# Performance work log

Measured on AMD Instinct MI355X. Metric: run time of the kernel, lower is better.

Reference implementation:

```python
import jax, jax.numpy as jnp
import numpy as np

B = 32768   # batch
D = 64      # latent_dimension_half
H = 256     # inner_dimension
T = D * (D + 1) // 2  # 2080 triangular outputs


def setup_inputs() -> dict:
    key = jax.random.key(0)
    ks = jax.random.split(key, 7)
    s = 0.05
    return {
        "x": jax.random.normal(ks[0], (B, D), dtype=jnp.float32),
        "W1": jax.random.normal(ks[1], (D, H), dtype=jnp.float32) * s,
        "b1": jax.random.normal(ks[2], (H,), dtype=jnp.float32) * s,
        "W2": jax.random.normal(ks[3], (H, H), dtype=jnp.float32) * s,
        "b2": jax.random.normal(ks[4], (H,), dtype=jnp.float32) * s,
        "W3": jax.random.normal(ks[5], (H, T), dtype=jnp.float32) * s,
        "b3": jax.random.normal(ks[6], (T,), dtype=jnp.float32) * s,
    }


def reference(x, W1, b1, W2, b2, W3, b3):
    d = x.shape[-1]  # latent_dimension_half
    h = jnp.tanh(x @ W1 + b1)
    h = jnp.tanh(h @ W2 + b2)
    t = jnp.tanh(h @ W3 + b3)  # [B, d*(d+1)/2]
    # scatter: first d entries -> diagonal (diagflat), rest -> strict upper
    # triangle in row-major order (matches torch boolean-mask assignment)
    di = np.arange(d)
    iu, ju = np.triu_indices(d, k=1)
    rows = np.concatenate([di, iu])
    cols = np.concatenate([di, ju])
    u = jnp.zeros((x.shape[0], d, d), dtype=t.dtype).at[:, rows, cols].set(t)
    # y[b] = u[b].T @ u[b]
    return jnp.einsum('bki,bkj->bij', u, u)
```

## Files before the change

kernel.cpp:

```cpp
#include <hip/hip_runtime.h>


typedef __bf16 bf16_t;
typedef bf16_t bf16x8 __attribute__((ext_vector_type(8)));
typedef float  f32x4  __attribute__((ext_vector_type(4)));

#define MFMA16(a, b, c) __builtin_amdgcn_mfma_f32_16x16x32_bf16((a), (b), (c), 0, 0, 0)

constexpr int SLOT  = 4608;
constexpr int H2OFF = 73728;

__device__ __forceinline__ float fast_tanh(float x) {
  float cx = fminf(fmaxf(x, -30.0f), 30.0f);
  float t  = __expf(2.0f * cx);
  return (t - 1.0f) * __builtin_amdgcn_rcpf(t + 1.0f);
}

__device__ __forceinline__ bf16x8 zsel(bf16x8 f, bool keep) {
  union { bf16x8 v; unsigned int u[4]; } x;
  x.v = f;
  unsigned m = keep ? 0xFFFFFFFFu : 0u;
#pragma unroll
  for (int p = 0; p < 4; ++p) x.u[p] &= m;
  return x.v;
}

__device__ __forceinline__ void decode_p(int p, int& j, int& k) {
  int cc = p >> 3, e = p & 7;
  int b = 0;
  while (b < 7 && cc >= 4 * (b + 1) * (b + 2)) ++b;
  int rl  = b + 1;
  int rem = cc - 4 * b * (b + 1);
  j = 8 * b + rem / rl;
  k = (rem % rl) * 8 + e;
}

__global__ void prep_kernel(const float* __restrict__ W1, const float* __restrict__ W2,
                            const float* __restrict__ W3, const float* __restrict__ b3,
                            char* __restrict__ wsb) {
  int tid = blockIdx.x * 512 + threadIdx.x;
  bf16_t* ws = (bf16_t*)wsb;
  if (tid < 16384) {
    int n = tid >> 6, k = tid & 63;
    ws[tid] = (bf16_t)W1[k * 256 + n];
  } else if (tid < 81920) {
    int m = tid - 16384;
    int n = m >> 8, k = m & 255;
    ws[tid] = (bf16_t)W2[k * 256 + n];
  } else if (tid < 671744) {
    int m = tid - 81920;
    int t  = m >> 12;
    int r  = m & 4095;
    int kk = r >> 9;
    int g  = (r >> 7) & 3;
    int c  = (r >> 3) & 15;
    int e  = r & 7;
    int p  = t * 16 + c;
    int k  = kk * 32 + g * 8 + e;
    int j, kd;
    decode_p(p, j, kd);
    float v = 0.f;
    if (kd <= j) {
      int n_ref = (kd == j) ? j : (64 + kd * 63 - (kd * (kd - 1)) / 2 + j - kd - 1);
      v = W3[k * 2080 + n_ref];
    }
    ws[tid] = (bf16_t)v;
  } else if (tid < 674048) {
    int p = tid - 671744;
    int j, kd;
    decode_p(p, j, kd);
    float v = 0.f;
    if (kd <= j) {
      int n_ref = (kd == j) ? j : (64 + kd * 63 - (kd * (kd - 1)) / 2 + j - kd - 1);
      v = b3[n_ref];
    }
    ((float*)(wsb + 1343488))[p] = v;
  }
}

__global__ void __launch_bounds__(512, 4)
hm_kernel(const float* __restrict__ x, const float* __restrict__ b1,
          const float* __restrict__ b2, const char* __restrict__ wsb,
          float* __restrict__ out) {
  extern __shared__ char smem[];
  const int tid  = threadIdx.x;
  const int w    = tid >> 6;
  const int lane = tid & 63;
  const int g    = lane >> 4;
  const int c    = lane & 15;
  const int blk  = blockIdx.x;

  const bf16_t* W1t = (const bf16_t*)wsb;
  const bf16_t* W2t = W1t + 16384;
  const bf16_t* W3q = W1t + 81920;
  const float*  b3p = (const float*)(wsb + 1343488);

  char* xs  = smem;
  char* h1s = smem + 8192;
  char* h2s = smem + H2OFF;

  if (tid < 256) {
    f32x4 v = *(const f32x4*)(x + (size_t)blk * 1024 + tid * 4);
    int row = tid >> 4, col = (tid & 15) * 4;
    union { bf16_t b[4]; unsigned long long u; } pk;
    pk.b[0] = (bf16_t)v[0]; pk.b[1] = (bf16_t)v[1];
    pk.b[2] = (bf16_t)v[2]; pk.b[3] = (bf16_t)v[3];
    *(unsigned long long*)(xs + ((row * 128 + col * 2) ^ ((row & 7) << 4))) = pk.u;
  }
  __syncthreads();

  {
    bf16x8 a0 = *(const bf16x8*)(xs + ((c * 128 + g * 16) ^ ((c & 7) << 4)));
    bf16x8 a1 = *(const bf16x8*)(xs + ((c * 128 + 64 + g * 16) ^ ((c & 7) << 4)));
#pragma unroll
    for (int ni = 0; ni < 2; ++ni) {
      int n = (w * 2 + ni) * 16 + c;
      bf16x8 bw0 = *(const bf16x8*)(W1t + n * 64 + g * 8);
      bf16x8 bw1 = *(const bf16x8*)(W1t + n * 64 + 32 + g * 8);
      f32x4 acc = {0.f, 0.f, 0.f, 0.f};
      acc = MFMA16(a0, bw0, acc);
      acc = MFMA16(a1, bw1, acc);
      float bias = b1[n];
#pragma unroll
      for (int r = 0; r < 4; ++r) {
        int row = g * 4 + r;
        float v = fast_tanh(acc[r] + bias);
        *(bf16_t*)(h1s + ((row * 512 + n * 2) ^ ((row & 7) << 4))) = (bf16_t)v;
      }
    }
  }
  __syncthreads();

#pragma unroll
  for (int ni = 0; ni < 2; ++ni) {
    int n = (w * 2 + ni) * 16 + c;
    f32x4 acc0 = {0.f, 0.f, 0.f, 0.f}, acc1 = {0.f, 0.f, 0.f, 0.f};
#pragma unroll
    for (int kk = 0; kk < 8; kk += 2) {
      bf16x8 a0 = *(const bf16x8*)(h1s + ((c * 512 + kk * 64 + g * 16) ^ ((c & 7) << 4)));
      bf16x8 a1 = *(const bf16x8*)(h1s + ((c * 512 + (kk + 1) * 64 + g * 16) ^ ((c & 7) << 4)));
      bf16x8 bw0 = *(const bf16x8*)(W2t + n * 256 + kk * 32 + g * 8);
      bf16x8 bw1 = *(const bf16x8*)(W2t + n * 256 + (kk + 1) * 32 + g * 8);
      acc0 = MFMA16(a0, bw0, acc0);
      acc1 = MFMA16(a1, bw1, acc1);
    }
    f32x4 acc = acc0 + acc1;
    float bias = b2[n];
#pragma unroll
    for (int r = 0; r < 4; ++r) {
      int row = g * 4 + r;
      float v = fast_tanh(acc[r] + bias);
      *(bf16_t*)(h2s + ((row * 512 + n * 2) ^ ((row & 7) << 4))) = (bf16_t)v;
    }
  }
  __syncthreads();

  {
    bf16x8 a0 = *(const bf16x8*)(h2s + ((c * 512 + 0 * 64 + g * 16) ^ ((c & 7) << 4)));
    bf16x8 a1 = *(const bf16x8*)(h2s + ((c * 512 + 1 * 64 + g * 16) ^ ((c & 7) << 4)));
    bf16x8 a2 = *(const bf16x8*)(h2s + ((c * 512 + 2 * 64 + g * 16) ^ ((c & 7) << 4)));
    bf16x8 a3 = *(const bf16x8*)(h2s + ((c * 512 + 3 * 64 + g * 16) ^ ((c & 7) << 4)));
    bf16x8 a4 = *(const bf16x8*)(h2s + ((c * 512 + 4 * 64 + g * 16) ^ ((c & 7) << 4)));
    bf16x8 a5 = *(const bf16x8*)(h2s + ((c * 512 + 5 * 64 + g * 16) ^ ((c & 7) << 4)));
    bf16x8 a6 = *(const bf16x8*)(h2s + ((c * 512 + 6 * 64 + g * 16) ^ ((c & 7) << 4)));
    bf16x8 a7 = *(const bf16x8*)(h2s + ((c * 512 + 7 * 64 + g * 16) ^ ((c & 7) << 4)));

    char* tw = smem + (g * 4) * SLOT;
    const int swz = (g & 7) << 4;

    bf16x8 A0, A1, A2, A3, A4, A5, A6, A7; float Ab;
    bf16x8 B0, B1, B2, B3, B4, B5, B6, B7; float Bb;

#define ISSUE_T(S, TI)                                                              \
  do {                                                                              \
    int t_ = w + (TI) * 8;                                                          \
    const bf16_t* np_ = W3q + t_ * 4096 + lane * 8;                                 \
    asm volatile("global_load_dwordx4 %0, %1, off" : "=v"(S##0) : "v"(np_));            \
    asm volatile("global_load_dwordx4 %0, %1, off" : "=v"(S##1) : "v"(np_ + 512));      \
    asm volatile("global_load_dwordx4 %0, %1, off" : "=v"(S##2) : "v"(np_ + 1024));     \
    asm volatile("global_load_dwordx4 %0, %1, off" : "=v"(S##3) : "v"(np_ + 1536));     \
    asm volatile("global_load_dwordx4 %0, %1, off" : "=v"(S##4) : "v"(np_ + 2048));     \
    asm volatile("global_load_dwordx4 %0, %1, off" : "=v"(S##5) : "v"(np_ + 2560));     \
    asm volatile("global_load_dwordx4 %0, %1, off" : "=v"(S##6) : "v"(np_ + 3072));     \
    asm volatile("global_load_dwordx4 %0, %1, off" : "=v"(S##7) : "v"(np_ + 3584));     \
    asm volatile("global_load_dword %0, %1, off"   : "=v"(S##b) : "v"(b3p + t_ * 16 + c)); \
  } while (0)

#define WAIT_N(N)                                          \
  do {                                                     \
    asm volatile("s_waitcnt vmcnt(" #N ")" ::: "memory");  \
    __builtin_amdgcn_sched_barrier(0);                     \
  } while (0)

#define COMP_T(S, TI)                                                    \
  do {                                                                   \
    f32x4 acc0 = {S##b, S##b, S##b, S##b};                               \
    f32x4 acc1 = {0.f, 0.f, 0.f, 0.f};                                   \
    acc0 = MFMA16(a0, S##0, acc0); acc1 = MFMA16(a1, S##1, acc1);        \
    acc0 = MFMA16(a2, S##2, acc0); acc1 = MFMA16(a3, S##3, acc1);        \
    acc0 = MFMA16(a4, S##4, acc0); acc1 = MFMA16(a5, S##5, acc1);        \
    acc0 = MFMA16(a6, S##6, acc0); acc1 = MFMA16(a7, S##7, acc1);        \
    f32x4 accs = acc0 + acc1;                                            \
    int p_ = (w + (TI) * 8) * 16 + c;                                    \
    _Pragma("unroll")                                                    \
    for (int r_ = 0; r_ < 4; ++r_) {                                     \
      float v_ = fast_tanh(accs[r_]);                                    \
      *(bf16_t*)(tw + r_ * SLOT + ((p_ * 2) ^ swz)) = (bf16_t)v_;        \
    }                                                                    \
  } while (0)

    ISSUE_T(A, 0);
#pragma unroll 1
    for (int pr = 0; pr < 8; ++pr) {
      ISSUE_T(B, 2 * pr + 1);
      WAIT_N(9);
      COMP_T(A, 2 * pr);
      ISSUE_T(A, 2 * pr + 2);
      WAIT_N(9);
      COMP_T(B, 2 * pr + 1);
    }
    ISSUE_T(B, 17);
    WAIT_N(9);
    COMP_T(A, 16);
    WAIT_N(0);
    COMP_T(B, 17);

#undef ISSUE_T
#undef WAIT_N
#undef COMP_T
  }
  __syncthreads();

#pragma unroll
  for (int bi = 0; bi < 2; ++bi) {
    int m = w * 2 + bi;
    char* slot = smem + m * SLOT;
    const int sw = ((m >> 2) & 7) << 4;

    bf16x8 f0, f1, f2, f3, f2b, f3b;
#pragma unroll
    for (int ti = 0; ti < 4; ++ti) {
      int j = ti * 16 + c;
      int Q = j >> 3, s = j & 7;
      int ro = 16 * (4 * Q * (Q + 1) + s * (Q + 1));
      bf16x8 fa = *(const bf16x8*)(slot + ((ro + g * 16) ^ sw));
      if (ti == 0) f0 = zsel(fa, g * 8 <= j);
      if (ti == 1) f1 = zsel(fa, g * 8 <= j);
      if (ti == 2) f2 = fa;
      if (ti == 3) f3 = fa;
      if (ti >= 2) {
        bf16x8 fb = *(const bf16x8*)(slot + ((ro + 64 + g * 16) ^ sw));
        fb = zsel(fb, 32 + g * 8 <= j);
        if (ti == 2) f2b = fb;
        else         f3b = fb;
      }
    }

    bf16x8 fA[4] = {f0, f1, f2, f3};
    f32x4 acc[4][4];
#pragma unroll
    for (int ti = 0; ti < 4; ++ti)
#pragma unroll
      for (int tj = 0; tj < 4; ++tj) {
        f32x4 z = {0.f, 0.f, 0.f, 0.f};
        acc[ti][tj] = MFMA16(fA[ti], fA[tj], z);
      }
    acc[2][2] = MFMA16(f2b, f2b, acc[2][2]);
    acc[2][3] = MFMA16(f2b, f3b, acc[2][3]);
    acc[3][2] = MFMA16(f3b, f2b, acc[3][2]);
    acc[3][3] = MFMA16(f3b, f3b, acc[3][3]);

    float* yb = out + (size_t)(blk * 16 + m) * 4096;
#pragma unroll
    for (int ti = 0; ti < 4; ++ti) {
#pragma unroll
      for (int tj = 0; tj < 4; ++tj)
#pragma unroll
        for (int r = 0; r < 4; ++r)
          *(float*)(slot + (g * 4 + r) * 256 + (tj * 16 + c) * 4) = acc[ti][tj][r];
#pragma unroll
      for (int ii = 0; ii < 4; ++ii) {
        f32x4 v = *(const f32x4*)(slot + ii * 1024 + lane * 16);
        *(f32x4*)(yb + ti * 1024 + ii * 256 + lane * 4) = v;
      }
    }
  }
}

extern "C" void kernel_launch(void* const* d_in, const int* in_sizes, int n_in,
                              void* d_out, int out_size, void* d_ws, size_t ws_size,
                              hipStream_t stream) {
  (void)in_sizes; (void)n_in; (void)out_size; (void)ws_size;
  const float* x  = (const float*)d_in[0];
  const float* W1 = (const float*)d_in[1];
  const float* b1 = (const float*)d_in[2];
  const float* W2 = (const float*)d_in[3];
  const float* b2 = (const float*)d_in[4];
  const float* W3 = (const float*)d_in[5];
  const float* b3 = (const float*)d_in[6];
  char* wsb = (char*)d_ws;
  float* out = (float*)d_out;

  prep_kernel<<<1317, 512, 0, stream>>>(W1, W2, W3, b3, wsb);

  hipFuncSetAttribute((const void*)hm_kernel,
                      hipFuncAttributeMaxDynamicSharedMemorySize, 81920);
  hm_kernel<<<2048, 512, 81920, stream>>>(x, b1, b2, wsb, out);
}
```

Baseline: 191.3 us.

## Make blocks persistent over 8 row tiles and overlap Gram output with next MLP

Each block now handles 8 tiles of 16 rows, where before it handled one. The launch drops from 2048 to 256 blocks, and two shared-memory arenas are double-buffered. The Gram product and output store for the previous tile are interleaved into the W3 load/MFMA loop of the current tile, so the large output write overlaps compute. Output stores become nontemporal, and biases are loaded once per block. Shared memory grows to 152KB and the launch bound occupancy drops to 2. With only 256 blocks, each CU may hold a single block, which reduces latency hiding.

```diff
diff --git a/kernel.cpp b/kernel.cpp
--- a/kernel.cpp
+++ b/kernel.cpp
@@ -8,7 +8,8 @@
 #define MFMA16(a, b, c) __builtin_amdgcn_mfma_f32_16x16x32_bf16((a), (b), (c), 0, 0, 0)
 
 constexpr int SLOT  = 4608;
-constexpr int H2OFF = 73728;
+constexpr int ARENA = 73728;
+constexpr int H2OFF = 147456;
 
 __device__ __forceinline__ float fast_tanh(float x) {
   float cx = fminf(fmaxf(x, -30.0f), 30.0f);
@@ -78,7 +79,57 @@
   }
 }
 
-__global__ void __launch_bounds__(512, 4)
+__device__ __forceinline__ void gram_store(char* slot, int sw, float* yb,
+                                           int g, int c, int lane) {
+  bf16x8 f0, f1, f2, f3, f2b, f3b;
+#pragma unroll
+  for (int ti = 0; ti < 4; ++ti) {
+    int j = ti * 16 + c;
+    int Q = j >> 3, s = j & 7;
+    int ro = 16 * (4 * Q * (Q + 1) + s * (Q + 1));
+    bf16x8 fa = *(const bf16x8*)(slot + ((ro + g * 16) ^ sw));
+    if (ti == 0) f0 = zsel(fa, g * 8 <= j);
+    if (ti == 1) f1 = zsel(fa, g * 8 <= j);
+    if (ti == 2) f2 = fa;
+    if (ti == 3) f3 = fa;
+    if (ti >= 2) {
+      bf16x8 fb = *(const bf16x8*)(slot + ((ro + 64 + g * 16) ^ sw));
+      fb = zsel(fb, 32 + g * 8 <= j);
+      if (ti == 2) f2b = fb;
+      else         f3b = fb;
+    }
+  }
+
+  bf16x8 fA[4] = {f0, f1, f2, f3};
+  f32x4 acc[4][4];
+#pragma unroll
+  for (int ti = 0; ti < 4; ++ti)
+#pragma unroll
+    for (int tj = 0; tj < 4; ++tj) {
+      f32x4 z = {0.f, 0.f, 0.f, 0.f};
+      acc[ti][tj] = MFMA16(fA[ti], fA[tj], z);
+    }
+  acc[2][2] = MFMA16(f2b, f2b, acc[2][2]);
+  acc[2][3] = MFMA16(f2b, f3b, acc[2][3]);
+  acc[3][2] = MFMA16(f3b, f2b, acc[3][2]);
+  acc[3][3] = MFMA16(f3b, f3b, acc[3][3]);
+
+#pragma unroll
+  for (int ti = 0; ti < 4; ++ti) {
+#pragma unroll
+    for (int tj = 0; tj < 4; ++tj)
+#pragma unroll
+      for (int r = 0; r < 4; ++r)
+        *(float*)(slot + (g * 4 + r) * 256 + (tj * 16 + c) * 4) = acc[ti][tj][r];
+#pragma unroll
+    for (int ii = 0; ii < 4; ++ii) {
+      f32x4 v = *(const f32x4*)(slot + ii * 1024 + lane * 16);
+      __builtin_nontemporal_store(v, (f32x4*)(yb + ti * 1024 + ii * 256 + lane * 4));
+    }
+  }
+}
+
+__global__ void __launch_bounds__(512, 2)
 hm_kernel(const float* __restrict__ x, const float* __restrict__ b1,
           const float* __restrict__ b2, const char* __restrict__ wsb,
           float* __restrict__ out) {
@@ -94,82 +145,92 @@
   const bf16_t* W2t = W1t + 16384;
   const bf16_t* W3q = W1t + 81920;
   const float*  b3p = (const float*)(wsb + 1343488);
-
-  char* xs  = smem;
-  char* h1s = smem + 8192;
   char* h2s = smem + H2OFF;
 
-  if (tid < 256) {
-    f32x4 v = *(const f32x4*)(x + (size_t)blk * 1024 + tid * 4);
-    int row = tid >> 4, col = (tid & 15) * 4;
-    union { bf16_t b[4]; unsigned long long u; } pk;
-    pk.b[0] = (bf16_t)v[0]; pk.b[1] = (bf16_t)v[1];
-    pk.b[2] = (bf16_t)v[2]; pk.b[3] = (bf16_t)v[3];
-    *(unsigned long long*)(xs + ((row * 128 + col * 2) ^ ((row & 7) << 4))) = pk.u;
-  }
-  __syncthreads();
-
-  {
-    bf16x8 a0 = *(const bf16x8*)(xs + ((c * 128 + g * 16) ^ ((c & 7) << 4)));
-    bf16x8 a1 = *(const bf16x8*)(xs + ((c * 128 + 64 + g * 16) ^ ((c & 7) << 4)));
+  float bias1[2], bias2[2];
+#pragma unroll
+  for (int ni = 0; ni < 2; ++ni) {
+    int n = (w * 2 + ni) * 16 + c;
+    bias1[ni] = b1[n];
+    bias2[ni] = b2[n];
+  }
+
+#pragma unroll 1
+  for (int r = 0; r < 8; ++r) {
+    char* cur = smem + (r & 1) * ARENA;
+    char* prv = smem + ((r & 1) ^ 1) * ARENA;
+    char* xs  = cur;
+    char* h1s = cur + 4096;
+
+    if (tid < 256) {
+      f32x4 v = *(const f32x4*)(x + ((size_t)blk * 128 + r * 16) * 64 + tid * 4);
+      int row = tid >> 4, col = (tid & 15) * 4;
+      union { bf16_t b[4]; unsigned long long u; } pk;
+      pk.b[0] = (bf16_t)v[0]; pk.b[1] = (bf16_t)v[1];
+      pk.b[2] = (bf16_t)v[2]; pk.b[3] = (bf16_t)v[3];
+      *(unsigned long long*)(xs + ((row * 128 + col * 2) ^ ((row & 7) << 4))) = pk.u;
+    }
+    __syncthreads();
+
+    {
+      bf16x8 a0 = *(const bf16x8*)(xs + ((c * 128 + g * 16) ^ ((c & 7) << 4)));
+      bf16x8 a1 = *(const bf16x8*)(xs + ((c * 128 + 64 + g * 16) ^ ((c & 7) << 4)));
+#pragma unroll
+      for (int ni = 0; ni < 2; ++ni) {
+        int n = (w * 2 + ni) * 16 + c;
+        bf16x8 bw0 = *(const bf16x8*)(W1t + n * 64 + g * 8);
+        bf16x8 bw1 = *(const bf16x8*)(W1t + n * 64 + 32 + g * 8);
+        f32x4 acc = {0.f, 0.f, 0.f, 0.f};
+        acc = MFMA16(a0, bw0, acc);
+        acc = MFMA16(a1, bw1, acc);
+#pragma unroll
+        for (int rr = 0; rr < 4; ++rr) {
+          int row = g * 4 + rr;
+          float v = fast_tanh(acc[rr] + bias1[ni]);
+          *(bf16_t*)(h1s + ((row * 512 + n * 2) ^ ((row & 7) << 4))) = (bf16_t)v;
+        }
+      }
+    }
+    __syncthreads();
+
 #pragma unroll
     for (int ni = 0; ni < 2; ++ni) {
       int n = (w * 2 + ni) * 16 + c;
-      bf16x8 bw0 = *(const bf16x8*)(W1t + n * 64 + g * 8);
-      bf16x8 bw1 = *(const bf16x8*)(W1t + n * 64 + 32 + g * 8);
-      f32x4 acc = {0.f, 0.f, 0.f, 0.f};
-      acc = MFMA16(a0, bw0, acc);
-      acc = MFMA16(a1, bw1, acc);
-      float bias = b1[n];
-#pragma unroll
-      for (int r = 0; r < 4; ++r) {
-        int row = g * 4 + r;
-        float v = fast_tanh(acc[r] + bias);
-        *(bf16_t*)(h1s + ((row * 512 + n * 2) ^ ((row & 7) << 4))) = (bf16_t)v;
+      f32x4 acc0 = {0.f, 0.f, 0.f, 0.f}, acc1 = {0.f, 0.f, 0.f, 0.f};
+#pragma unroll
+      for (int kk = 0; kk < 8; kk += 2) {
+        bf16x8 a0 = *(const bf16x8*)(h1s + ((c * 512 + kk * 64 + g * 16) ^ ((c & 7) << 4)));
+        bf16x8 a1 = *(const bf16x8*)(h1s + ((c * 512 + (kk + 1) * 64 + g * 16) ^ ((c & 7) << 4)));
+        bf16x8 bw0 = *(const bf16x8*)(W2t + n * 256 + kk * 32 + g * 8);
+        bf16x8 bw1 = *(const bf16x8*)(W2t + n * 256 + (kk + 1) * 32 + g * 8);
+        acc0 = MFMA16(a0, bw0, acc0);
+        acc1 = MFMA16(a1, bw1, acc1);
       }
-    }
-  }
-  __syncthreads();
-
-#pragma unroll
-  for (int ni = 0; ni < 2; ++ni) {
-    int n = (w * 2 + ni) * 16 + c;
-    f32x4 acc0 = {0.f, 0.f, 0.f, 0.f}, acc1 = {0.f, 0.f, 0.f, 0.f};
-#pragma unroll
-    for (int kk = 0; kk < 8; kk += 2) {
-      bf16x8 a0 = *(const bf16x8*)(h1s + ((c * 512 + kk * 64 + g * 16) ^ ((c & 7) << 4)));
-      bf16x8 a1 = *(const bf16x8*)(h1s + ((c * 512 + (kk + 1) * 64 + g * 16) ^ ((c & 7) << 4)));
-      bf16x8 bw0 = *(const bf16x8*)(W2t + n * 256 + kk * 32 + g * 8);
-      bf16x8 bw1 = *(const bf16x8*)(W2t + n * 256 + (kk + 1) * 32 + g * 8);
-      acc0 = MFMA16(a0, bw0, acc0);
-      acc1 = MFMA16(a1, bw1, acc1);
-    }
-    f32x4 acc = acc0 + acc1;
-    float bias = b2[n];
-#pragma unroll
-    for (int r = 0; r < 4; ++r) {
-      int row = g * 4 + r;
-      float v = fast_tanh(acc[r] + bias);
-      *(bf16_t*)(h2s + ((row * 512 + n * 2) ^ ((row & 7) << 4))) = (bf16_t)v;
-    }
-  }
-  __syncthreads();
-
-  {
-    bf16x8 a0 = *(const bf16x8*)(h2s + ((c * 512 + 0 * 64 + g * 16) ^ ((c & 7) << 4)));
-    bf16x8 a1 = *(const bf16x8*)(h2s + ((c * 512 + 1 * 64 + g * 16) ^ ((c & 7) << 4)));
-    bf16x8 a2 = *(const bf16x8*)(h2s + ((c * 512 + 2 * 64 + g * 16) ^ ((c & 7) << 4)));
-    bf16x8 a3 = *(const bf16x8*)(h2s + ((c * 512 + 3 * 64 + g * 16) ^ ((c & 7) << 4)));
-    bf16x8 a4 = *(const bf16x8*)(h2s + ((c * 512 + 4 * 64 + g * 16) ^ ((c & 7) << 4)));
-    bf16x8 a5 = *(const bf16x8*)(h2s + ((c * 512 + 5 * 64 + g * 16) ^ ((c & 7) << 4)));
-    bf16x8 a6 = *(const bf16x8*)(h2s + ((c * 512 + 6 * 64 + g * 16) ^ ((c & 7) << 4)));
-    bf16x8 a7 = *(const bf16x8*)(h2s + ((c * 512 + 7 * 64 + g * 16) ^ ((c & 7) << 4)));
-
-    char* tw = smem + (g * 4) * SLOT;
-    const int swz = (g & 7) << 4;
-
-    bf16x8 A0, A1, A2, A3, A4, A5, A6, A7; float Ab;
-    bf16x8 B0, B1, B2, B3, B4, B5, B6, B7; float Bb;
+      f32x4 acc = acc0 + acc1;
+#pragma unroll
+      for (int rr = 0; rr < 4; ++rr) {
+        int row = g * 4 + rr;
+        float v = fast_tanh(acc[rr] + bias2[ni]);
+        *(bf16_t*)(h2s + ((row * 512 + n * 2) ^ ((row & 7) << 4))) = (bf16_t)v;
+      }
+    }
+    __syncthreads();
+
+    {
+      bf16x8 a0 = *(const bf16x8*)(h2s + ((c * 512 + 0 * 64 + g * 16) ^ ((c & 7) << 4)));
+      bf16x8 a1 = *(const bf16x8*)(h2s + ((c * 512 + 1 * 64 + g * 16) ^ ((c & 7) << 4)));
+      bf16x8 a2 = *(const bf16x8*)(h2s + ((c * 512 + 2 * 64 + g * 16) ^ ((c & 7) << 4)));
+      bf16x8 a3 = *(const bf16x8*)(h2s + ((c * 512 + 3 * 64 + g * 16) ^ ((c & 7) << 4)));
+      bf16x8 a4 = *(const bf16x8*)(h2s + ((c * 512 + 4 * 64 + g * 16) ^ ((c & 7) << 4)));
+      bf16x8 a5 = *(const bf16x8*)(h2s + ((c * 512 + 5 * 64 + g * 16) ^ ((c & 7) << 4)));
+      bf16x8 a6 = *(const bf16x8*)(h2s + ((c * 512 + 6 * 64 + g * 16) ^ ((c & 7) << 4)));
+      bf16x8 a7 = *(const bf16x8*)(h2s + ((c * 512 + 7 * 64 + g * 16) ^ ((c & 7) << 4)));
+
+      char* tw = cur + (g * 4) * SLOT;
+      const int swz = (g & 7) << 4;
+
+      bf16x8 A0, A1, A2, A3, A4, A5, A6, A7; float Ab;
+      bf16x8 B0, B1, B2, B3, B4, B5, B6, B7; float Bb;
 
 #define ISSUE_T(S, TI)                                                              \
   do {                                                                              \
@@ -209,81 +270,42 @@
     }                                                                    \
   } while (0)
 
-    ISSUE_T(A, 0);
+      ISSUE_T(A, 0);
 #pragma unroll 1
-    for (int pr = 0; pr < 8; ++pr) {
-      ISSUE_T(B, 2 * pr + 1);
+      for (int pr = 0; pr < 8; ++pr) {
+        ISSUE_T(B, 2 * pr + 1);
+        WAIT_N(9);
+        COMP_T(A, 2 * pr);
+        ISSUE_T(A, 2 * pr + 2);
+        WAIT_N(9);
+        COMP_T(B, 2 * pr + 1);
+        if (r > 0 && (pr == 1 || pr == 5)) {
+          int bi = (pr == 5);
+          int m  = w * 2 + bi;
+          gram_store(prv + m * SLOT, ((m >> 2) & 7) << 4,
+                     out + ((size_t)blk * 128 + (r - 1) * 16 + m) * 4096,
+                     g, c, lane);
+        }
+      }
+      ISSUE_T(B, 17);
       WAIT_N(9);
-      COMP_T(A, 2 * pr);
-      ISSUE_T(A, 2 * pr + 2);
-      WAIT_N(9);
-      COMP_T(B, 2 * pr + 1);
-    }
-    ISSUE_T(B, 17);
-    WAIT_N(9);
-    COMP_T(A, 16);
-    WAIT_N(0);
-    COMP_T(B, 17);
+      COMP_T(A, 16);
+      WAIT_N(0);
+      COMP_T(B, 17);
 
 #undef ISSUE_T
 #undef WAIT_N
 #undef COMP_T
-  }
-  __syncthreads();
+    }
+    __syncthreads();
+  }
 
 #pragma unroll
   for (int bi = 0; bi < 2; ++bi) {
     int m = w * 2 + bi;
-    char* slot = smem + m * SLOT;
-    const int sw = ((m >> 2) & 7) << 4;
-
-    bf16x8 f0, f1, f2, f3, f2b, f3b;
-#pragma unroll
-    for (int ti = 0; ti < 4; ++ti) {
-      int j = ti * 16 + c;
-      int Q = j >> 3, s = j & 7;
-      int ro = 16 * (4 * Q * (Q + 1) + s * (Q + 1));
-      bf16x8 fa = *(const bf16x8*)(slot + ((ro + g * 16) ^ sw));
-      if (ti == 0) f0 = zsel(fa, g * 8 <= j);
-      if (ti == 1) f1 = zsel(fa, g * 8 <= j);
-      if (ti == 2) f2 = fa;
-      if (ti == 3) f3 = fa;
-      if (ti >= 2) {
-        bf16x8 fb = *(const bf16x8*)(slot + ((ro + 64 + g * 16) ^ sw));
-        fb = zsel(fb, 32 + g * 8 <= j);
-        if (ti == 2) f2b = fb;
-        else         f3b = fb;
-      }
-    }
-
-    bf16x8 fA[4] = {f0, f1, f2, f3};
-    f32x4 acc[4][4];
-#pragma unroll
-    for (int ti = 0; ti < 4; ++ti)
-#pragma unroll
-      for (int tj = 0; tj < 4; ++tj) {
-        f32x4 z = {0.f, 0.f, 0.f, 0.f};
-        acc[ti][tj] = MFMA16(fA[ti], fA[tj], z);
-      }
-    acc[2][2] = MFMA16(f2b, f2b, acc[2][2]);
-    acc[2][3] = MFMA16(f2b, f3b, acc[2][3]);
-    acc[3][2] = MFMA16(f3b, f2b, acc[3][2]);
-    acc[3][3] = MFMA16(f3b, f3b, acc[3][3]);
-
-    float* yb = out + (size_t)(blk * 16 + m) * 4096;
-#pragma unroll
-    for (int ti = 0; ti < 4; ++ti) {
-#pragma unroll
-      for (int tj = 0; tj < 4; ++tj)
-#pragma unroll
-        for (int r = 0; r < 4; ++r)
-          *(float*)(slot + (g * 4 + r) * 256 + (tj * 16 + c) * 4) = acc[ti][tj][r];
-#pragma unroll
-      for (int ii = 0; ii < 4; ++ii) {
-        f32x4 v = *(const f32x4*)(slot + ii * 1024 + lane * 16);
-        *(f32x4*)(yb + ti * 1024 + ii * 256 + lane * 4) = v;
-      }
-    }
+    gram_store(smem + ARENA + m * SLOT, ((m >> 2) & 7) << 4,
+               out + ((size_t)blk * 128 + 7 * 16 + m) * 4096,
+               g, c, lane);
   }
 }
 
@@ -304,6 +326,6 @@
   prep_kernel<<<1317, 512, 0, stream>>>(W1, W2, W3, b3, wsb);
 
   hipFuncSetAttribute((const void*)hm_kernel,
-                      hipFuncAttributeMaxDynamicSharedMemorySize, 81920);
-  hm_kernel<<<2048, 512, 81920, stream>>>(x, b1, b2, wsb, out);
-}
+                      hipFuncAttributeMaxDynamicSharedMemorySize, 155648);
+  hm_kernel<<<256, 512, 155648, stream>>>(x, b1, b2, wsb, out);
+}
```

Measured after the change: 181.6 us. 5.1% less time.
